# Optimization experiments

Measured on AMD Instinct MI355X. Metric: run time of the kernel, lower is better.

## Reference

```python
import jax, jax.numpy as jnp
import numpy as np
import math
from jax.scipy.special import logsumexp

T, S, M, D = 2048, 128, 8, 64


def setup_inputs() -> dict:
    key = jax.random.key(0)
    k1, k2, k3, k4, k5 = jax.random.split(key, 5)
    return {
        "X": jax.random.normal(k1, (T, D), jnp.float32),
        "pi_logits": 0.1 * jax.random.normal(k2, (S,), jnp.float32),
        "trans_logits": 0.1 * jax.random.normal(k3, (S, S), jnp.float32),
        "weight_logits": 0.1 * jax.random.normal(k4, (S, M), jnp.float32),
        "means": jax.random.normal(k5, (S, M, D), jnp.float32),
        "log_vars": jnp.zeros((S, M, D), jnp.float32),
    }


def reference(X, pi_logits, trans_logits, weight_logits, means, log_vars):
    t, d = X.shape
    # GMM emission log-probs: diagonal Gaussians per (state, mixture)
    diff = X[:, None, None, :] - means[None]                    # [T,S,M,D]
    inv_vars = jnp.exp(-log_vars)                               # [S,M,D]
    exp_term = -0.5 * jnp.sum(diff * diff * inv_vars[None], axis=3)  # [T,S,M]
    log_norm = -0.5 * (jnp.sum(log_vars, axis=2) + d * math.log(2 * math.pi))  # [S,M]
    comp_log_prob = exp_term + log_norm[None]                   # [T,S,M]
    log_mix_w = jax.nn.log_softmax(weight_logits, axis=1)       # [S,M]
    emission_log_prob = logsumexp(comp_log_prob + log_mix_w[None], axis=2)  # [T,S]

    log_pi = jax.nn.log_softmax(pi_logits, axis=0)              # [S]
    log_A = jax.nn.log_softmax(trans_logits, axis=1)            # [S,S]

    alpha0 = log_pi + emission_log_prob[0]                      # [S]

    def step(prev, em_t):
        # faithful to original: logsumexp over dim=1 of prev[:,None] + log_A
        new = em_t + logsumexp(prev[:, None] + log_A, axis=1)
        return new, None

    alpha_last, _ = jax.lax.scan(step, alpha0, emission_log_prob[1:])
    return logsumexp(alpha_last, axis=0)
```

## Files before the change

### kernel.cpp

```cpp
#include <hip/hip_runtime.h>
#include <hip/hip_bf16.h>
#include <math.h>

#define LOG2PI 1.8378770664093453f

typedef __attribute__((ext_vector_type(8))) short bf16x8;
typedef __attribute__((ext_vector_type(4))) float f32x4;

__device__ __forceinline__ ushort f2bf(float f) {
    __hip_bfloat16 h = __float2bfloat16(f);
    return *reinterpret_cast<ushort*>(&h);
}


__global__ __launch_bounds__(1024) void emis_mfma_kernel(
    const float* __restrict__ X,
    const float* __restrict__ means,
    const float* __restrict__ log_vars,
    const float* __restrict__ weight_logits,
    const float* __restrict__ trans_logits,
    float* __restrict__ part,
    float* __restrict__ base) {
    __shared__ __align__(16) char A_l[128 * 256];
    __shared__ __align__(16) char B_l[64 * 256];
    __shared__ float soff_l[64];
    __shared__ float wred[16][4];

    const int tb = blockIdx.x & 15;
    const int sc = blockIdx.x >> 4;
    const int tid = threadIdx.x;
    const int w  = tid >> 6;
    const int ln = tid & 63;
    const int wr = w & 7;
    const int wc = w >> 3;
    const int t0 = tb * 128;

    {
        const float4* Xv = (const float4*)(X + (size_t)t0 * 64);
        #pragma unroll
        for (int p = 0; p < 2; p++) {
            int g  = p * 1024 + tid;
            int r  = g >> 4;
            int d4 = g & 15;
            float4 x = Xv[g];
            int swz = (r & 7) << 4;
            ushort4 sq = { f2bf(x.x * x.x), f2bf(x.y * x.y),
                           f2bf(x.z * x.z), f2bf(x.w * x.w) };
            ushort4 xl = { f2bf(x.x), f2bf(x.y), f2bf(x.z), f2bf(x.w) };
            *(ushort4*)(A_l + r * 256 + ((d4 * 8) ^ swz)) = sq;
            *(ushort4*)(A_l + r * 256 + ((128 + d4 * 8) ^ swz)) = xl;
        }
    }

    #pragma unroll
    for (int i = 0; i < 4; i++) {
        int n  = w * 4 + i;
        int gi = sc * 4096 + n * 64 + ln;
        float lv = log_vars[gi];
        float mu = means[gi];
        float iv = __expf(-lv);
        float bv = -2.0f * mu * iv;
        int swz = (n & 7) << 4;
        *(ushort*)(B_l + n * 256 + ((ln * 2) ^ swz))       = f2bf(iv);
        *(ushort*)(B_l + n * 256 + ((128 + ln * 2) ^ swz)) = f2bf(bv);
        float c = fmaf(mu * mu, iv, lv);
        #pragma unroll
        for (int o = 32; o > 0; o >>= 1) c += __shfl_xor(c, o, 64);
        if (ln == 0)
            soff_l[n] = -0.5f * (c + 64.0f * LOG2PI);
    }

    if (tb == 0 && w >= 8) {
        int sg = sc * 8 + (w - 8);
        const float* tr = trans_logits + sg * 128;
        float v0 = tr[ln], v1 = tr[ln + 64];
        float m = fmaxf(v0, v1);
        #pragma unroll
        for (int o = 32; o > 0; o >>= 1) m = fmaxf(m, __shfl_xor(m, o, 64));
        float sum = __expf(v0 - m) + __expf(v1 - m);
        #pragma unroll
        for (int o = 32; o > 0; o >>= 1) sum += __shfl_xor(sum, o, 64);
        float L = m + __logf(sum);
        float C = (m - L) + __logf(sum);
        if (ln == 0) base[sg] = 2047.0f * C;
    }
    __syncthreads();

    if (tid < 64) {
        float wl = weight_logits[sc * 64 + tid];
        float wm = wl;
        #pragma unroll
        for (int o = 1; o < 8; o <<= 1) wm = fmaxf(wm, __shfl_xor(wm, o, 64));
        float we = __expf(wl - wm);
        float ws = we;
        #pragma unroll
        for (int o = 1; o < 8; o <<= 1) ws += __shfl_xor(ws, o, 64);
        soff_l[tid] += wl - (wm + __logf(ws));
    }

    const int lr = ln & 15;
    const int lg = ln >> 4;
    const int n0 = wc * 32;
    f32x4 acc[2];
    #pragma unroll
    for (int ct = 0; ct < 2; ct++) acc[ct] = (f32x4){0.f, 0.f, 0.f, 0.f};

    #pragma unroll
    for (int kk = 0; kk < 4; kk++) {
        const int kb = kk * 64 + lg * 16;
        int t = wr * 16 + lr;
        bf16x8 af = *(const bf16x8*)(A_l + t * 256 + (kb ^ ((t & 7) << 4)));
        #pragma unroll
        for (int ct = 0; ct < 2; ct++) {
            int n = n0 + ct * 16 + lr;
            bf16x8 bfr = *(const bf16x8*)(B_l + n * 256 + (kb ^ ((n & 7) << 4)));
            acc[ct] = __builtin_amdgcn_mfma_f32_16x16x32_bf16(af, bfr, acc[ct], 0, 0, 0);
        }
    }
    __syncthreads();

    float so[2];
    #pragma unroll
    for (int ct = 0; ct < 2; ct++) so[ct] = soff_l[n0 + ct * 16 + lr];

    float psum[2] = {0.f, 0.f};
    #pragma unroll
    for (int ct = 0; ct < 2; ct++) {
        #pragma unroll
        for (int r = 0; r < 4; r++) {
            float v = fmaf(-0.5f, acc[ct][r], so[ct]);
            float mx = v;
            mx = fmaxf(mx, __shfl_xor(mx, 1, 64));
            mx = fmaxf(mx, __shfl_xor(mx, 2, 64));
            mx = fmaxf(mx, __shfl_xor(mx, 4, 64));
            float e = __expf(v - mx);
            e += __shfl_xor(e, 1, 64);
            e += __shfl_xor(e, 2, 64);
            e += __shfl_xor(e, 4, 64);
            psum[ct] += mx + __logf(e);
        }
    }
    #pragma unroll
    for (int ct = 0; ct < 2; ct++) {
        psum[ct] += __shfl_xor(psum[ct], 16, 64);
        psum[ct] += __shfl_xor(psum[ct], 32, 64);
    }
    if ((ln & 7) == 0 && ln < 16) {
        #pragma unroll
        for (int ct = 0; ct < 2; ct++)
            wred[w][ct * 2 + (ln >> 3)] = psum[ct];
    }
    __syncthreads();

    if (tid < 8) {
        int wbase = (tid >> 2) * 8;
        int slot  = tid & 3;
        float v = 0.f;
        #pragma unroll
        for (int r = 0; r < 8; r++) v += wred[wbase + r][slot];
        part[(sc * 8 + tid) * 16 + tb] = v;
    }
}

__global__ void final_kernel(const float* __restrict__ part,
                             const float* __restrict__ base,
                             const float* __restrict__ pi_logits,
                             float* __restrict__ out) {
    __shared__ float smx[2], ssum[2], amx[2], asum[2];
    int tid = threadIdx.x;
    int wv = tid >> 6, ln = tid & 63;

    float p = pi_logits[tid];
    float mx = p;
    #pragma unroll
    for (int o = 32; o > 0; o >>= 1) mx = fmaxf(mx, __shfl_xor(mx, o, 64));
    if (ln == 0) smx[wv] = mx;
    __syncthreads();
    float gmx = fmaxf(smx[0], smx[1]);
    float e = __expf(p - gmx);
    #pragma unroll
    for (int o = 32; o > 0; o >>= 1) e += __shfl_xor(e, o, 64);
    if (ln == 0) ssum[wv] = e;
    __syncthreads();
    float lsepi = gmx + __logf(ssum[0] + ssum[1]);

    float v = 0.f;
    const float4* p4 = (const float4*)(part + tid * 16);
    #pragma unroll
    for (int j = 0; j < 4; j++) {
        float4 a = p4[j];
        v += ((a.x + a.y) + (a.z + a.w));
    }
    float alpha = (p - lsepi) + base[tid] + v;

    float m2 = alpha;
    #pragma unroll
    for (int o = 32; o > 0; o >>= 1) m2 = fmaxf(m2, __shfl_xor(m2, o, 64));
    if (ln == 0) amx[wv] = m2;
    __syncthreads();
    float g2 = fmaxf(amx[0], amx[1]);
    float e2 = __expf(alpha - g2);
    #pragma unroll
    for (int o = 32; o > 0; o >>= 1) e2 += __shfl_xor(e2, o, 64);
    if (ln == 0) asum[wv] = e2;
    __syncthreads();
    if (tid == 0) out[0] = g2 + __logf(asum[0] + asum[1]);
}

extern "C" void kernel_launch(void* const* d_in, const int* in_sizes, int n_in,
                              void* d_out, int out_size, void* d_ws, size_t ws_size,
                              hipStream_t stream) {
    const float* X      = (const float*)d_in[0];
    const float* pi_l   = (const float*)d_in[1];
    const float* trans  = (const float*)d_in[2];
    const float* weight = (const float*)d_in[3];
    const float* means  = (const float*)d_in[4];
    const float* lvars  = (const float*)d_in[5];
    float* out = (float*)d_out;

    float* ws_part = (float*)d_ws;
    float* ws_base = ws_part + 2048;

    emis_mfma_kernel<<<256, 1024, 0, stream>>>(X, means, lvars, weight, trans,
                                               ws_part, ws_base);
    final_kernel<<<1, 128, 0, stream>>>(ws_part, ws_base, pi_l, out);
}
```

Baseline: 14.98 us.

## Fold per-component offset into MFMA and merge final logsumexp reductions

Instead of reducing mu^2*iv+lv across 64 lanes with shuffles per component, the sum is stored as bf16 in a new LDS tile and added into the accumulators by extra MFMAs against an all-ones operand. This removes the shuffle reductions and one __syncthreads, and the weight log-softmax now runs before the first barrier. The final kernel computes the pi and alpha logsumexps in parallel by subtracting lse(pi) at the end, cutting the barrier count from four to two. The bf16 rounding of the per-dimension offset terms adds some precision loss.

```diff
diff --git a/kernel.cpp b/kernel.cpp
--- a/kernel.cpp
+++ b/kernel.cpp
@@ -23,6 +23,7 @@
     float* __restrict__ base) {
     __shared__ __align__(16) char A_l[128 * 256];
     __shared__ __align__(16) char B_l[64 * 256];
+    __shared__ __align__(16) char B2_l[64 * 128];
     __shared__ float soff_l[64];
     __shared__ float wred[16][4];
 
@@ -59,15 +60,22 @@
         float lv = log_vars[gi];
         float mu = means[gi];
         float iv = __expf(-lv);
-        float bv = -2.0f * mu * iv;
         int swz = (n & 7) << 4;
-        *(ushort*)(B_l + n * 256 + ((ln * 2) ^ swz))       = f2bf(iv);
-        *(ushort*)(B_l + n * 256 + ((128 + ln * 2) ^ swz)) = f2bf(bv);
-        float c = fmaf(mu * mu, iv, lv);
-        #pragma unroll
-        for (int o = 32; o > 0; o >>= 1) c += __shfl_xor(c, o, 64);
-        if (ln == 0)
-            soff_l[n] = -0.5f * (c + 64.0f * LOG2PI);
+        *(ushort*)(B_l  + n * 256 + ((ln * 2) ^ swz))       = f2bf(iv);
+        *(ushort*)(B_l  + n * 256 + ((128 + ln * 2) ^ swz)) = f2bf(-2.0f * mu * iv);
+        *(ushort*)(B2_l + n * 128 + ((ln * 2) ^ swz))       = f2bf(fmaf(mu * mu, iv, lv));
+    }
+
+    if (tid < 64) {
+        float wl = weight_logits[sc * 64 + tid];
+        float wm = wl;
+        #pragma unroll
+        for (int o = 1; o < 8; o <<= 1) wm = fmaxf(wm, __shfl_xor(wm, o, 64));
+        float we = __expf(wl - wm);
+        float ws = we;
+        #pragma unroll
+        for (int o = 1; o < 8; o <<= 1) ws += __shfl_xor(ws, o, 64);
+        soff_l[tid] = (wl - (wm + __logf(ws))) - 32.0f * LOG2PI;
     }
 
     if (tb == 0 && w >= 8) {
@@ -86,30 +94,23 @@
     }
     __syncthreads();
 
-    if (tid < 64) {
-        float wl = weight_logits[sc * 64 + tid];
-        float wm = wl;
-        #pragma unroll
-        for (int o = 1; o < 8; o <<= 1) wm = fmaxf(wm, __shfl_xor(wm, o, 64));
-        float we = __expf(wl - wm);
-        float ws = we;
-        #pragma unroll
-        for (int o = 1; o < 8; o <<= 1) ws += __shfl_xor(ws, o, 64);
-        soff_l[tid] += wl - (wm + __logf(ws));
-    }
-
     const int lr = ln & 15;
     const int lg = ln >> 4;
+    const int tA = wr * 16 + lr;
     const int n0 = wc * 32;
+    const int aswz = (tA & 7) << 4;
+    bf16x8 ones;
+    #pragma unroll
+    for (int j = 0; j < 8; j++) ones[j] = (short)0x3F80;
+
     f32x4 acc[2];
-    #pragma unroll
-    for (int ct = 0; ct < 2; ct++) acc[ct] = (f32x4){0.f, 0.f, 0.f, 0.f};
+    acc[0] = (f32x4){0.f, 0.f, 0.f, 0.f};
+    acc[1] = (f32x4){0.f, 0.f, 0.f, 0.f};
 
     #pragma unroll
     for (int kk = 0; kk < 4; kk++) {
         const int kb = kk * 64 + lg * 16;
-        int t = wr * 16 + lr;
-        bf16x8 af = *(const bf16x8*)(A_l + t * 256 + (kb ^ ((t & 7) << 4)));
+        bf16x8 af = *(const bf16x8*)(A_l + tA * 256 + (kb ^ aswz));
         #pragma unroll
         for (int ct = 0; ct < 2; ct++) {
             int n = n0 + ct * 16 + lr;
@@ -117,7 +118,16 @@
             acc[ct] = __builtin_amdgcn_mfma_f32_16x16x32_bf16(af, bfr, acc[ct], 0, 0, 0);
         }
     }
-    __syncthreads();
+    #pragma unroll
+    for (int kk = 0; kk < 2; kk++) {
+        const int kb = kk * 64 + lg * 16;
+        #pragma unroll
+        for (int ct = 0; ct < 2; ct++) {
+            int n = n0 + ct * 16 + lr;
+            bf16x8 bfr = *(const bf16x8*)(B2_l + n * 128 + (kb ^ ((n & 7) << 4)));
+            acc[ct] = __builtin_amdgcn_mfma_f32_16x16x32_bf16(ones, bfr, acc[ct], 0, 0, 0);
+        }
+    }
 
     float so[2];
     #pragma unroll
@@ -166,24 +176,11 @@
                              const float* __restrict__ base,
                              const float* __restrict__ pi_logits,
                              float* __restrict__ out) {
-    __shared__ float smx[2], ssum[2], amx[2], asum[2];
+    __shared__ float pm[2], qm[2], ps[2], qs[2];
     int tid = threadIdx.x;
     int wv = tid >> 6, ln = tid & 63;
 
     float p = pi_logits[tid];
-    float mx = p;
-    #pragma unroll
-    for (int o = 32; o > 0; o >>= 1) mx = fmaxf(mx, __shfl_xor(mx, o, 64));
-    if (ln == 0) smx[wv] = mx;
-    __syncthreads();
-    float gmx = fmaxf(smx[0], smx[1]);
-    float e = __expf(p - gmx);
-    #pragma unroll
-    for (int o = 32; o > 0; o >>= 1) e += __shfl_xor(e, o, 64);
-    if (ln == 0) ssum[wv] = e;
-    __syncthreads();
-    float lsepi = gmx + __logf(ssum[0] + ssum[1]);
-
     float v = 0.f;
     const float4* p4 = (const float4*)(part + tid * 16);
     #pragma unroll
@@ -191,20 +188,32 @@
         float4 a = p4[j];
         v += ((a.x + a.y) + (a.z + a.w));
     }
-    float alpha = (p - lsepi) + base[tid] + v;
-
-    float m2 = alpha;
-    #pragma unroll
-    for (int o = 32; o > 0; o >>= 1) m2 = fmaxf(m2, __shfl_xor(m2, o, 64));
-    if (ln == 0) amx[wv] = m2;
-    __syncthreads();
-    float g2 = fmaxf(amx[0], amx[1]);
-    float e2 = __expf(alpha - g2);
-    #pragma unroll
-    for (int o = 32; o > 0; o >>= 1) e2 += __shfl_xor(e2, o, 64);
-    if (ln == 0) asum[wv] = e2;
-    __syncthreads();
-    if (tid == 0) out[0] = g2 + __logf(asum[0] + asum[1]);
+    float q = p + base[tid] + v;
+
+    float mp = p, mq = q;
+    #pragma unroll
+    for (int o = 32; o > 0; o >>= 1) {
+        mp = fmaxf(mp, __shfl_xor(mp, o, 64));
+        mq = fmaxf(mq, __shfl_xor(mq, o, 64));
+    }
+    if (ln == 0) { pm[wv] = mp; qm[wv] = mq; }
+    __syncthreads();
+    float gp = fmaxf(pm[0], pm[1]);
+    float gq = fmaxf(qm[0], qm[1]);
+    float ep = __expf(p - gp);
+    float eq = __expf(q - gq);
+    #pragma unroll
+    for (int o = 32; o > 0; o >>= 1) {
+        ep += __shfl_xor(ep, o, 64);
+        eq += __shfl_xor(eq, o, 64);
+    }
+    if (ln == 0) { ps[wv] = ep; qs[wv] = eq; }
+    __syncthreads();
+    if (tid == 0) {
+        float lsep = gp + __logf(ps[0] + ps[1]);
+        float lseq = gq + __logf(qs[0] + qs[1]);
+        out[0] = lseq - lsep;
+    }
 }
 
 extern "C" void kernel_launch(void* const* d_in, const int* in_sizes, int n_in,
```

Result: faster. 13.57 us (-9.4%).
